# Kernel tuning notes

Measured on AMD Instinct MI355X. Metric: run time of the kernel, lower is better.

## Reference

```python
import jax, jax.numpy as jnp
import numpy as np

P, C, L, D_IN, F = 200000, 50000, 8, 64, 32


def gru_step(x, h, Wi, Wh, bi, bh):
    # torch nn.GRU single-layer cell math. Wi, Wh: [3F, F]; bi, bh: [3F]
    gi = x @ Wi.T + bi
    gh = h @ Wh.T + bh
    i_r, i_z, i_n = jnp.split(gi, 3, axis=-1)
    h_r, h_z, h_n = jnp.split(gh, 3, axis=-1)
    r = jax.nn.sigmoid(i_r + h_r)
    z = jax.nn.sigmoid(i_z + h_z)
    n = jnp.tanh(i_n + r * h_n)
    return (1.0 - z) * n + z * h


def setup_inputs() -> dict:
    key = jax.random.key(0)
    ks = jax.random.split(key, 16)
    s = 0.1
    return {
        "path_raw": jax.random.normal(ks[0], (P, D_IN), jnp.float32),
        "channel_raw": jax.random.normal(ks[1], (C, D_IN), jnp.float32),
        "path_channel_idx": jax.random.randint(ks[2], (P, L), 0, C),
        "path_lengths": jax.random.randint(ks[3], (P,), 0, L),  # valid length = lengths+1 in [1, L]
        "num_steps": 5,
        "W_path_init": s * jax.random.normal(ks[4], (D_IN, F), jnp.float32),
        "b_path_init": jnp.zeros((F,), jnp.float32),
        "W_chan_init": s * jax.random.normal(ks[5], (D_IN, F), jnp.float32),
        "b_chan_init": jnp.zeros((F,), jnp.float32),
        "Wi1": s * jax.random.normal(ks[6], (3 * F, F), jnp.float32),
        "Wh1": s * jax.random.normal(ks[7], (3 * F, F), jnp.float32),
        "bi1": jnp.zeros((3 * F,), jnp.float32),
        "bh1": jnp.zeros((3 * F,), jnp.float32),
        "Wi2": s * jax.random.normal(ks[8], (3 * F, F), jnp.float32),
        "Wh2": s * jax.random.normal(ks[9], (3 * F, F), jnp.float32),
        "bi2": jnp.zeros((3 * F,), jnp.float32),
        "bh2": jnp.zeros((3 * F,), jnp.float32),
    }


def reference(path_raw, channel_raw, path_channel_idx, path_lengths, num_steps,
              W_path_init, b_path_init, W_chan_init, b_chan_init,
              Wi1, Wh1, bi1, bh1, Wi2, Wh2, bi2, bh2):
    # Initialization: Linear + ReLU on raw padded features
    p = jax.nn.relu(path_raw @ W_path_init + b_path_init)      # [P, F]
    c = jax.nn.relu(channel_raw @ W_chan_init + b_chan_init)   # [C, F]

    # mask[p, t] = 1 if slot t is a real channel on path p (lengths in 1..L)
    mask = (jnp.arange(L)[None, :] <= path_lengths[:, None]).astype(p.dtype)  # [P, L]
    flat_idx = path_channel_idx.reshape(-1)                    # [P*L]

    for _ in range(num_steps):
        # --- GRUCell1: each path runs its channel sequence through a GRU,
        # with the path feature as the evolving hidden state. Batched over
        # all paths; masked positions keep the previous hidden state.
        def body(h, t):
            x = c[path_channel_idx[:, t]]                      # [P, F] gather
            h_new = gru_step(x, h, Wi1, Wh1, bi1, bh1)
            m = mask[:, t][:, None]
            return m * h_new + (1.0 - m) * h, None

        p, _ = jax.lax.scan(body, p, jnp.arange(L))

        # --- GRUCell2: each channel sums the features of paths containing it,
        # then does one GRU step with that sum as input, channel feat as hidden.
        contrib = (p[:, None, :] * mask[:, :, None]).reshape(P * L, F)
        agg = jax.ops.segment_sum(contrib, flat_idx, num_segments=C)  # [C, F]
        c = gru_step(agg, c, Wi2, Wh2, bi2, bh2)

    return p, c
```

## Files before the change

### kernel.cpp

```cpp
#include <hip/hip_runtime.h>

#define DIN 64
#define FF 32
#define MAX_OUTER 8
#define NCH 3

__device__ __forceinline__ float sigm(float x) {
  return 1.0f / (1.0f + __expf(-x));
}
__device__ __forceinline__ float tanh_fast(float x) {
  float e = __expf(2.0f * x);
  return 1.0f - 2.0f / (e + 1.0f);
}

template <int K>
__device__ __forceinline__ void swz_fma3(float h,
                                         const float* __restrict__ wr,
                                         const float* __restrict__ wz,
                                         const float* __restrict__ wn,
                                         float& ar, float& az, float& an) {
  if constexpr (K < FF) {
    float hk = __int_as_float(
        __builtin_amdgcn_ds_swizzle(__float_as_int(h), (K << 5)));
    ar = fmaf(hk, wr[K], ar);
    az = fmaf(hk, wz[K], az);
    an = fmaf(hk, wn[K], an);
    swz_fma3<K + 1>(h, wr, wz, wn, ar, az, an);
  }
}

template <int K, int NC>
__device__ __forceinline__ void swz_fma_multi(
    const float* __restrict__ h,
    const float* __restrict__ wr, const float* __restrict__ wz,
    const float* __restrict__ wn,
    float* __restrict__ ar, float* __restrict__ az, float* __restrict__ an) {
  if constexpr (K < FF) {
    float hk[NC];
#pragma unroll
    for (int c = 0; c < NC; ++c)
      hk[c] = __int_as_float(
          __builtin_amdgcn_ds_swizzle(__float_as_int(h[c]), (K << 5)));
#pragma unroll
    for (int c = 0; c < NC; ++c) {
      ar[c] = fmaf(hk[c], wr[K], ar[c]);
      az[c] = fmaf(hk[c], wz[K], az[c]);
      an[c] = fmaf(hk[c], wn[K], an[c]);
    }
    swz_fma_multi<K + 1, NC>(h, wr, wz, wn, ar, az, an);
  }
}

__device__ __forceinline__ int iread(const void* src, long i, int is64) {
  return is64 ? (int)((const long long*)src)[i] : ((const int*)src)[i];
}

__global__ void detect_dtypes(const int* __restrict__ idx_raw,
                              const int* __restrict__ lens_raw,
                              int* __restrict__ flags) {
  __shared__ int zi, zl;
  if (threadIdx.x == 0) { zi = 0; zl = 0; }
  __syncthreads();
  int j = threadIdx.x;
  if (idx_raw[2 * j + 1] == 0)  atomicAdd(&zi, 1);
  if (lens_raw[2 * j + 1] == 0) atomicAdd(&zl, 1);
  __syncthreads();
  if (threadIdx.x == 0) {
    flags[0] = (zi >= 250) ? 1 : 0;
    flags[1] = (zl >= 250) ? 1 : 0;
  }
}

__device__ __forceinline__ void gru_gates(
    const float* __restrict__ Wi, const float* __restrict__ Wh,
    const float* __restrict__ bi, const float* __restrict__ bh,
    const float* __restrict__ x, float* __restrict__ h) {
  float hn[FF];
#pragma unroll
  for (int g = 0; g < FF; ++g) {
    float ar   = bi[g] + bh[g];
    float az   = bi[FF + g] + bh[FF + g];
    float an_i = bi[2 * FF + g];
    float an_h = bh[2 * FF + g];
#pragma unroll
    for (int k = 0; k < FF; ++k) {
      const float xk = x[k];
      const float hk = h[k];
      ar   = fmaf(xk, Wi[g * FF + k], ar);
      ar   = fmaf(hk, Wh[g * FF + k], ar);
      az   = fmaf(xk, Wi[(FF + g) * FF + k], az);
      az   = fmaf(hk, Wh[(FF + g) * FF + k], az);
      an_i = fmaf(xk, Wi[(2 * FF + g) * FF + k], an_i);
      an_h = fmaf(hk, Wh[(2 * FF + g) * FF + k], an_h);
    }
    float r = sigm(ar);
    float z = sigm(az);
    float n = tanh_fast(fmaf(r, an_h, an_i));
    hn[g] = fmaf(z, h[g] - n, n);
  }
#pragma unroll
  for (int g = 0; g < FF; ++g) h[g] = hn[g];
}

__global__ __launch_bounds__(256) void init_proj(
    const float* __restrict__ raw,
    const float* __restrict__ W, const float* __restrict__ b,
    float* __restrict__ out, int nrows) {
  int i = blockIdx.x * blockDim.x + threadIdx.x;
  if (i >= nrows) return;
  float x[DIN];
  const float4* rp = (const float4*)(raw + (size_t)i * DIN);
#pragma unroll
  for (int q = 0; q < DIN / 4; ++q) {
    float4 v = rp[q];
    x[q * 4 + 0] = v.x; x[q * 4 + 1] = v.y; x[q * 4 + 2] = v.z; x[q * 4 + 3] = v.w;
  }
  float acc[FF];
#pragma unroll
  for (int j = 0; j < FF; ++j) acc[j] = b[j];
#pragma unroll
  for (int k = 0; k < DIN; ++k) {
    float xk = x[k];
#pragma unroll
    for (int j = 0; j < FF; ++j) acc[j] = fmaf(xk, W[k * FF + j], acc[j]);
  }
  float4* op = (float4*)(out + (size_t)i * FF);
#pragma unroll
  for (int j = 0; j < FF; j += 4) {
    float4 v;
    v.x = fmaxf(acc[j + 0], 0.0f);
    v.y = fmaxf(acc[j + 1], 0.0f);
    v.z = fmaxf(acc[j + 2], 0.0f);
    v.w = fmaxf(acc[j + 3], 0.0f);
    op[j / 4] = v;
  }
}


__global__ __launch_bounds__(256) void path_pre(
    const void* __restrict__ idx_raw, const void* __restrict__ lens_raw,
    const int* __restrict__ flags, int* __restrict__ cnt,
    int* __restrict__ lhist, int P, int C, int L) {
  __shared__ int bh[72];
  const int nb = L + 1;
  if (threadIdx.x < nb) bh[threadIdx.x] = 0;
  __syncthreads();
  int i = blockIdx.x * blockDim.x + threadIdx.x;
  if (i < P) {
    int i64 = flags[0], l64 = flags[1];
    int len = iread(lens_raw, i, l64);
    if (len > L - 1) len = L - 1;
    int lb = (len < 0) ? 0 : len;
    atomicAdd(&bh[lb], 1);
    for (int t = 0; t <= len; ++t) {
      int ch = iread(idx_raw, (long)i * L + t, i64);
      if (ch < 0) ch = 0;
      if (ch >= C) ch = C - 1;
      atomicAdd(&cnt[ch], 1);
    }
  }
  __syncthreads();
  if (threadIdx.x < nb && bh[threadIdx.x] > 0)
    atomicAdd(&lhist[threadIdx.x], bh[threadIdx.x]);
}

__global__ __launch_bounds__(1024) void scan_counts(
    const int* __restrict__ cnt, int* __restrict__ rowstart,
    int* __restrict__ cursor, int n) {
  __shared__ int buf[1024];
  __shared__ int carry;
  if (threadIdx.x == 0) carry = 0;
  __syncthreads();
  for (int base = 0; base < n; base += 1024) {
    int i = base + threadIdx.x;
    int v = (i < n) ? cnt[i] : 0;
    buf[threadIdx.x] = v;
    __syncthreads();
    for (int off = 1; off < 1024; off <<= 1) {
      int t = (threadIdx.x >= off) ? buf[threadIdx.x - off] : 0;
      __syncthreads();
      buf[threadIdx.x] += t;
      __syncthreads();
    }
    int excl = buf[threadIdx.x] - v;
    if (i < n) { rowstart[i] = carry + excl; cursor[i] = carry + excl; }
    __syncthreads();
    if (threadIdx.x == 0) carry += buf[1023];
    __syncthreads();
  }
  if (threadIdx.x == 0) rowstart[n] = carry;
}

__global__ __launch_bounds__(256) void fill_entries(
    const void* __restrict__ idx_raw, const void* __restrict__ lens_raw,
    const int* __restrict__ flags, int* __restrict__ cursor,
    int* __restrict__ entries, int P, int C, int L) {
  int i = blockIdx.x * blockDim.x + threadIdx.x;
  if (i >= P) return;
  int i64 = flags[0], l64 = flags[1];
  int len = iread(lens_raw, i, l64);
  if (len > L - 1) len = L - 1;
  for (int t = 0; t <= len; ++t) {
    int ch = iread(idx_raw, (long)i * L + t, i64);
    if (ch < 0) ch = 0;
    if (ch >= C) ch = C - 1;
    int slot = atomicAdd(&cursor[ch], 1);
    entries[slot] = i;
  }
}

__global__ __launch_bounds__(256) void fill_order2(
    const void* __restrict__ lens_raw, const int* __restrict__ flags,
    int* __restrict__ lcursor, int* __restrict__ order, int P, int L) {
  __shared__ int bh[72];
  __shared__ int bbase[72];
  const int nb = L + 1;
  if (threadIdx.x < nb) bh[threadIdx.x] = 0;
  __syncthreads();
  int i = blockIdx.x * blockDim.x + threadIdx.x;
  int lb = 0, rank = 0;
  if (i < P) {
    int len = iread(lens_raw, i, flags[1]);
    if (len > L - 1) len = L - 1;
    lb = (len < 0) ? 0 : len;
    rank = atomicAdd(&bh[lb], 1);
  }
  __syncthreads();
  if (threadIdx.x < nb && bh[threadIdx.x] > 0)
    bbase[threadIdx.x] = atomicAdd(&lcursor[threadIdx.x], bh[threadIdx.x]);
  __syncthreads();
  if (i < P) order[bbase[lb] + rank] = i;
}

__global__ __launch_bounds__(256) void build_sorted(
    const void* __restrict__ idx_raw, const void* __restrict__ lens_raw,
    const int* __restrict__ flags, const int* __restrict__ order,
    int* __restrict__ idx_s, int* __restrict__ len_s, int P, int C, int L) {
  int tid = blockIdx.x * blockDim.x + threadIdx.x;
  if (tid >= P) return;
  int i = order[tid];
  int i64 = flags[0], l64 = flags[1];
  int len = iread(lens_raw, i, l64);
  if (len > L - 1) len = L - 1;
  len_s[tid] = len;
  for (int t = 0; t < L; ++t) {
    int ch = iread(idx_raw, (long)i * L + t, i64);
    if (ch < 0) ch = 0;
    if (ch >= C) ch = C - 1;
    idx_s[(size_t)t * P + tid] = ch * (3 * FF * 4);
  }
}


__global__ __launch_bounds__(256) void gates_pre(
    const float* __restrict__ c_state,
    const float* __restrict__ Wi1, const float* __restrict__ bi1,
    const float* __restrict__ Wh2, const float* __restrict__ bh2,
    float* __restrict__ gi1, float* __restrict__ gh2, int C,
    const int* __restrict__ ns_ptr, int use_mem, int s) {
  int ns = use_mem ? *ns_ptr : 5;
  if (ns < 1 || ns > MAX_OUTER) ns = 5;
  if (s >= ns) return;
  int c = blockIdx.x * blockDim.x + threadIdx.x;
  if (c >= C) return;
  int q = blockIdx.y;
  int qq = (q < 3) ? q : q - 3;
  const float* W = ((q < 3) ? Wi1 : Wh2) + (size_t)qq * FF * FF;
  const float* b = ((q < 3) ? bi1 : bh2) + qq * FF;
  float* out = ((q < 3) ? gi1 : gh2) + (size_t)c * (3 * FF) + qq * FF;

  float x[FF];
  const float4* cp = (const float4*)(c_state + (size_t)c * FF);
#pragma unroll
  for (int t = 0; t < FF / 4; ++t) {
    float4 v = cp[t];
    x[4 * t + 0] = v.x; x[4 * t + 1] = v.y; x[4 * t + 2] = v.z; x[4 * t + 3] = v.w;
  }
  float acc[FF];
#pragma unroll
  for (int j = 0; j < FF; ++j) acc[j] = b[j];
#pragma unroll
  for (int k = 0; k < FF; ++k) {
    float xk = x[k];
#pragma unroll
    for (int j = 0; j < FF; ++j) acc[j] = fmaf(xk, W[(size_t)j * FF + k], acc[j]);
  }
  float4* op = (float4*)out;
#pragma unroll
  for (int j = 0; j < FF; j += 4) {
    float4 v; v.x = acc[j]; v.y = acc[j + 1]; v.z = acc[j + 2]; v.w = acc[j + 3];
    op[j / 4] = v;
  }
}

__global__ __launch_bounds__(256, 4) void path_step(
    const float* __restrict__ c_state, float* __restrict__ p_state,
    const void* __restrict__ idx_raw, const void* __restrict__ lens_raw,
    const int* __restrict__ flags, const int* __restrict__ order,
    const float* __restrict__ Wi, const float* __restrict__ Wh,
    const float* __restrict__ bi, const float* __restrict__ bh,
    int P, int C, int L, const int* __restrict__ ns_ptr, int use_mem, int s) {
  int ns = use_mem ? *ns_ptr : 5;
  if (ns < 1 || ns > MAX_OUTER) ns = 5;
  if (s >= ns) return;
  int tid = blockIdx.x * blockDim.x + threadIdx.x;
  if (tid >= P) return;
  int i = order[tid];
  int i64 = flags[0], l64 = flags[1];
  int len = iread(lens_raw, i, l64);
  if (len > L - 1) len = L - 1;

  float h[FF];
  const float4* pp = (const float4*)(p_state + (size_t)i * FF);
#pragma unroll
  for (int q = 0; q < FF / 4; ++q) {
    float4 v = pp[q];
    h[q * 4 + 0] = v.x; h[q * 4 + 1] = v.y; h[q * 4 + 2] = v.z; h[q * 4 + 3] = v.w;
  }

#pragma unroll 1
  for (int t = 0; t <= len && t < L; ++t) {
    int ch = iread(idx_raw, (long)i * L + t, i64);
    if (ch < 0) ch = 0;
    if (ch >= C) ch = C - 1;
    float x[FF];
    const float4* cp = (const float4*)(c_state + (size_t)ch * FF);
#pragma unroll
    for (int q = 0; q < FF / 4; ++q) {
      float4 v = cp[q];
      x[q * 4 + 0] = v.x; x[q * 4 + 1] = v.y; x[q * 4 + 2] = v.z; x[q * 4 + 3] = v.w;
    }
    gru_gates(Wi, Wh, bi, bh, x, h);
  }

  float4* op = (float4*)(p_state + (size_t)i * FF);
#pragma unroll
  for (int q = 0; q < FF / 4; ++q) {
    float4 v;
    v.x = h[q * 4 + 0]; v.y = h[q * 4 + 1]; v.z = h[q * 4 + 2]; v.w = h[q * 4 + 3];
    op[q] = v;
  }
}

__global__ __launch_bounds__(256, 3) void path_step6(
    const float* __restrict__ gi1,
    float* __restrict__ p_state,
    const int* __restrict__ idx_s,
    const int* __restrict__ len_s,
    const int* __restrict__ order,
    const float* __restrict__ Wh,
    const float* __restrict__ bh,
    int P, int L,
    const int* __restrict__ ns_ptr, int use_mem, int s) {
  int ns = use_mem ? *ns_ptr : 5;
  if (ns < 1 || ns > MAX_OUTER) ns = 5;
  if (s >= ns) return;
  const int lane = threadIdx.x & 63;
  const int g = lane & 31;
  const long wv = (long)blockIdx.x * (blockDim.x >> 6) + (threadIdx.x >> 6);
  const long base = wv * (2 * NCH);

  long pos[NCH];
  bool valid[NCH];
  int path[NCH], len[NCH];
#pragma unroll
  for (int c = 0; c < NCH; ++c) {
    pos[c] = base + 2 * c + (lane >> 5);
    valid[c] = pos[c] < P;
    if (!valid[c]) pos[c] = P - 1;
    path[c] = order[pos[c]];
    len[c] = valid[c] ? len_s[pos[c]] : -1;
  }

  float wr[FF], wz[FF], wn[FF];
  {
    const float4* a = (const float4*)(Wh + (size_t)g * FF);
    const float4* b = (const float4*)(Wh + (size_t)(FF + g) * FF);
    const float4* c = (const float4*)(Wh + (size_t)(2 * FF + g) * FF);
#pragma unroll
    for (int q = 0; q < FF / 4; ++q) {
      float4 va = a[q];
      wr[4 * q + 0] = va.x; wr[4 * q + 1] = va.y; wr[4 * q + 2] = va.z; wr[4 * q + 3] = va.w;
      float4 vb = b[q];
      wz[4 * q + 0] = vb.x; wz[4 * q + 1] = vb.y; wz[4 * q + 2] = vb.z; wz[4 * q + 3] = vb.w;
      float4 vc = c[q];
      wn[4 * q + 0] = vc.x; wn[4 * q + 1] = vc.y; wn[4 * q + 2] = vc.z; wn[4 * q + 3] = vc.w;
    }
  }
#pragma unroll
  for (int k = 0; k < FF; ++k) {
    asm volatile("" : "+v"(wr[k]), "+v"(wz[k]), "+v"(wn[k]));
  }
  const float bhr = bh[g], bhz = bh[FF + g], bhn = bh[2 * FF + g];

  float h[NCH];
#pragma unroll
  for (int c = 0; c < NCH; ++c) h[c] = p_state[(size_t)path[c] * FF + g];

  int lenM = len[0];
#pragma unroll
  for (int c = 1; c < NCH; ++c) lenM = (len[c] > lenM) ? len[c] : lenM;

  if (lenM >= 0) {
    const char* gB = (const char*)gi1 + (size_t)(4 * g);
    const int* row = idx_s;
    int off[NCH];
#pragma unroll
    for (int c = 0; c < NCH; ++c) off[c] = row[pos[c]];
    row += P;

#pragma unroll 1
    for (int t = 0; t <= lenM; ++t) {
      int offn[NCH];
#pragma unroll
      for (int c = 0; c < NCH; ++c)
        offn[c] = (t < lenM) ? row[pos[c]] : off[c];
      row += P;

      float gr[NCH], gz[NCH], gn[NCH];
#pragma unroll
      for (int c = 0; c < NCH; ++c) {
        const char* p = gB + off[c];
        gr[c] = *(const float*)(p);
        gz[c] = *(const float*)(p + 128);
        gn[c] = *(const float*)(p + 256);
      }

      float ar[NCH], az[NCH], an[NCH];
#pragma unroll
      for (int c = 0; c < NCH; ++c) { ar[c] = bhr; az[c] = bhz; an[c] = bhn; }
      swz_fma_multi<0, NCH>(h, wr, wz, wn, ar, az, an);

#pragma unroll
      for (int c = 0; c < NCH; ++c) {
        float r = sigm(gr[c] + ar[c]);
        float z = sigm(gz[c] + az[c]);
        float n = tanh_fast(fmaf(r, an[c], gn[c]));
        float hn_ = fmaf(z, h[c] - n, n);
        h[c] = (t <= len[c]) ? hn_ : h[c];
        off[c] = offn[c];
      }
    }
  }
#pragma unroll
  for (int c = 0; c < NCH; ++c)
    if (valid[c]) p_state[(size_t)path[c] * FF + g] = h[c];
}

__global__ __launch_bounds__(256) void agg_gather(
    const float* __restrict__ p_state, const int* __restrict__ rowstart,
    const int* __restrict__ entries, float* __restrict__ agg,
    int C, const int* __restrict__ ns_ptr, int use_mem, int s) {
  int ns = use_mem ? *ns_ptr : 5;
  if (ns < 1 || ns > MAX_OUTER) ns = 5;
  if (s >= ns) return;
  int c = blockIdx.x * 8 + (threadIdx.x >> 5);
  int j = threadIdx.x & 31;
  if (c >= C) return;
  int rs = rowstart[c], re = rowstart[c + 1];
  float acc = 0.0f, acc2 = 0.0f;
  int e = rs;
  for (; e + 1 < re; e += 2) {
    int p0 = entries[e], p1 = entries[e + 1];
    acc  += p_state[(size_t)p0 * FF + j];
    acc2 += p_state[(size_t)p1 * FF + j];
  }
  if (e < re) acc += p_state[(size_t)entries[e] * FF + j];
  agg[(size_t)c * FF + j] = acc + acc2;
}

__global__ __launch_bounds__(256) void chan_step(
    float* __restrict__ c_state, const float* __restrict__ agg,
    const float* __restrict__ Wi, const float* __restrict__ Wh,
    const float* __restrict__ bi, const float* __restrict__ bh,
    int C, const int* __restrict__ ns_ptr, int use_mem, int s) {
  int ns = use_mem ? *ns_ptr : 5;
  if (ns < 1 || ns > MAX_OUTER) ns = 5;
  if (s >= ns) return;
  int i = blockIdx.x * blockDim.x + threadIdx.x;
  if (i >= C) return;

  float x[FF], h[FF];
  const float4* apv = (const float4*)(agg + (size_t)i * FF);
  const float4* cpv = (const float4*)(c_state + (size_t)i * FF);
#pragma unroll
  for (int q = 0; q < FF / 4; ++q) {
    float4 a = apv[q];
    x[q * 4 + 0] = a.x; x[q * 4 + 1] = a.y; x[q * 4 + 2] = a.z; x[q * 4 + 3] = a.w;
    float4 c = cpv[q];
    h[q * 4 + 0] = c.x; h[q * 4 + 1] = c.y; h[q * 4 + 2] = c.z; h[q * 4 + 3] = c.w;
  }
  gru_gates(Wi, Wh, bi, bh, x, h);
  float4* op = (float4*)(c_state + (size_t)i * FF);
#pragma unroll
  for (int q = 0; q < FF / 4; ++q) {
    float4 v;
    v.x = h[q * 4 + 0]; v.y = h[q * 4 + 1]; v.z = h[q * 4 + 2]; v.w = h[q * 4 + 3];
    op[q] = v;
  }
}

__global__ __launch_bounds__(256, 3) void chan_fused(
    float* __restrict__ c_state, const float* __restrict__ p_state,
    const int* __restrict__ rowstart, const int* __restrict__ entries,
    const float* __restrict__ gh2,
    const float* __restrict__ Wi2, const float* __restrict__ bi2,
    int C, const int* __restrict__ ns_ptr, int use_mem, int s) {
  int ns = use_mem ? *ns_ptr : 5;
  if (ns < 1 || ns > MAX_OUTER) ns = 5;
  if (s >= ns) return;
  const int lane = threadIdx.x & 63;
  const int g = lane & 31;
  const long wv = (long)blockIdx.x * (blockDim.x >> 6) + (threadIdx.x >> 6);
  const long c = wv * 2 + (lane >> 5);
  if (c >= C) return;

  float wr[FF], wz[FF], wn[FF];
  {
    const float4* a = (const float4*)(Wi2 + (size_t)g * FF);
    const float4* b = (const float4*)(Wi2 + (size_t)(FF + g) * FF);
    const float4* d = (const float4*)(Wi2 + (size_t)(2 * FF + g) * FF);
#pragma unroll
    for (int q = 0; q < FF / 4; ++q) {
      float4 va = a[q];
      wr[4 * q + 0] = va.x; wr[4 * q + 1] = va.y; wr[4 * q + 2] = va.z; wr[4 * q + 3] = va.w;
      float4 vb = b[q];
      wz[4 * q + 0] = vb.x; wz[4 * q + 1] = vb.y; wz[4 * q + 2] = vb.z; wz[4 * q + 3] = vb.w;
      float4 vd = d[q];
      wn[4 * q + 0] = vd.x; wn[4 * q + 1] = vd.y; wn[4 * q + 2] = vd.z; wn[4 * q + 3] = vd.w;
    }
  }
  const float bir = bi2[g], biz = bi2[FF + g], bin_ = bi2[2 * FF + g];

  int rs = rowstart[c], re = rowstart[c + 1];
  float acc = 0.0f, acc2 = 0.0f;
  int e = rs;
  for (; e + 3 < re; e += 4) {
    int p0 = entries[e], p1 = entries[e + 1], p2 = entries[e + 2], p3 = entries[e + 3];
    acc  += p_state[(size_t)p0 * FF + g];
    acc2 += p_state[(size_t)p1 * FF + g];
    acc  += p_state[(size_t)p2 * FF + g];
    acc2 += p_state[(size_t)p3 * FF + g];
  }
  for (; e < re; ++e) acc += p_state[(size_t)entries[e] * FF + g];
  float x = acc + acc2;

  float ar = bir, az = biz, an = bin_;
  swz_fma3<0>(x, wr, wz, wn, ar, az, an);
  const float* pre = gh2 + (size_t)c * (3 * FF);
  float hr = pre[g], hz = pre[FF + g], hn = pre[2 * FF + g];
  float h = c_state[(size_t)c * FF + g];
  float r = sigm(ar + hr);
  float z = sigm(az + hz);
  float n = tanh_fast(fmaf(r, hn, an));
  c_state[(size_t)c * FF + g] = fmaf(z, h - n, n);
}

__global__ void beacon(float* out, int code) {
  out[0] = (float)(1024 * (64 + code));
}

extern "C" void kernel_launch(void* const* d_in, const int* in_sizes, int n_in,
                              void* d_out, int out_size, void* d_ws, size_t ws_size,
                              hipStream_t stream) {
  int base = 5, use_mem = 1;
  if (n_in == 16) { base = 4; use_mem = 0; }
  const float* path_raw = (const float*)d_in[0];
  const float* chan_raw = (const float*)d_in[1];
  const void* idx_raw  = d_in[2];
  const void* lens_raw = d_in[3];
  const int* ns_ptr = use_mem ? (const int*)d_in[4] : (const int*)d_in[0];
  const float* Wp  = (const float*)d_in[base + 0];
  const float* bp  = (const float*)d_in[base + 1];
  const float* Wc  = (const float*)d_in[base + 2];
  const float* bc  = (const float*)d_in[base + 3];
  const float* Wi1 = (const float*)d_in[base + 4];
  const float* Wh1 = (const float*)d_in[base + 5];
  const float* bi1 = (const float*)d_in[base + 6];
  const float* bh1 = (const float*)d_in[base + 7];
  const float* Wi2 = (const float*)d_in[base + 8];
  const float* Wh2 = (const float*)d_in[base + 9];
  const float* bi2 = (const float*)d_in[base + 10];
  const float* bh2 = (const float*)d_in[base + 11];

  long P = in_sizes[0] / DIN;
  long C = in_sizes[1] / DIN;
  long L = (P > 0) ? (in_sizes[2] / P) : 8;
  long PL = P * L;

  int anomaly = 0;
  if (n_in != 17 && n_in != 16) anomaly |= 1;
  if (P <= 0 || C <= 0 || L < 1 || L > 64) anomaly |= 2;
  if (P > 0 && in_sizes[3] != (int)P) anomaly |= 4;
  if ((long)out_size != (P + C) * FF) anomaly |= 8;

  float* out_f   = (float*)d_out;
  float* p_state = out_f;
  float* c_state = out_f + (size_t)P * FF;

  int* flags    = (int*)d_ws;
  int* rowstart = flags + 16;
  int* cursor   = rowstart + (C + 1);
  int* entries  = cursor + C;
  float* agg    = (float*)(entries + PL);
  int* order    = (int*)(agg + (size_t)C * FF);
  int* lhist    = order + P;
  int* lrow     = lhist + (L + 1);
  size_t base_words = (size_t)16 + (C + 1) + C + PL + (size_t)C * FF +
                      P + (L + 1) + (L + 2);
  size_t w1 = (base_words + 3) & ~(size_t)3;
  int* idx_s = (int*)d_ws + w1;
  int* len_s = idx_s + PL;
  size_t w2 = (w1 + (size_t)PL + P + 3) & ~(size_t)3;
  float* gi1 = (float*)d_ws + w2;
  float* gh2 = gi1 + (size_t)C * 3 * FF;
  size_t need_old = base_words * 4;
  size_t need_new = (w2 + (size_t)2 * C * 3 * FF) * 4;
  if (ws_size < need_old) anomaly |= 16;
  int use_new = (!anomaly) && (ws_size >= need_new) && (L >= 1) && (L <= 8) &&
                (C < 5000000);

  detect_dtypes<<<1, 256, 0, stream>>>((const int*)idx_raw, (const int*)lens_raw, flags);

  init_proj<<<(int)((P + 255) / 256), 256, 0, stream>>>(path_raw, Wp, bp, p_state, (int)P);
  init_proj<<<(int)((C + 255) / 256), 256, 0, stream>>>(chan_raw, Wc, bc, c_state, (int)C);

  (void)hipMemsetAsync(cursor, 0, (size_t)C * sizeof(int), stream);
  (void)hipMemsetAsync(lhist, 0, (size_t)(L + 1) * sizeof(int), stream);
  path_pre<<<(int)((P + 255) / 256), 256, 0, stream>>>(
      idx_raw, lens_raw, flags, cursor, lhist, (int)P, (int)C, (int)L);
  scan_counts<<<1, 1024, 0, stream>>>(cursor, rowstart, cursor, (int)C);
  fill_entries<<<(int)((P + 255) / 256), 256, 0, stream>>>(
      idx_raw, lens_raw, flags, cursor, entries, (int)P, (int)C, (int)L);
  scan_counts<<<1, 1024, 0, stream>>>(lhist, lrow, lhist, (int)L + 1);
  fill_order2<<<(int)((P + 255) / 256), 256, 0, stream>>>(
      lens_raw, flags, lhist, order, (int)P, (int)L);

  if (use_new) {
    build_sorted<<<(int)((P + 255) / 256), 256, 0, stream>>>(
        idx_raw, lens_raw, flags, order, idx_s, len_s, (int)P, (int)C, (int)L);
    const int paths_per_block = 4 * 2 * NCH;
    for (int s = 0; s < MAX_OUTER; ++s) {
      dim3 gpre((unsigned)((C + 255) / 256), 6, 1);
      gates_pre<<<gpre, 256, 0, stream>>>(
          c_state, Wi1, bi1, Wh2, bh2, gi1, gh2, (int)C, ns_ptr, use_mem, s);
      path_step6<<<(int)((P + paths_per_block - 1) / paths_per_block), 256, 0, stream>>>(
          gi1, p_state, idx_s, len_s, order, Wh1, bh1, (int)P, (int)L,
          ns_ptr, use_mem, s);
      chan_fused<<<(int)((C + 7) / 8), 256, 0, stream>>>(
          c_state, p_state, rowstart, entries, gh2, Wi2, bi2, (int)C,
          ns_ptr, use_mem, s);
    }
  } else {
    for (int s = 0; s < MAX_OUTER; ++s) {
      path_step<<<(int)((P + 255) / 256), 256, 0, stream>>>(
          c_state, p_state, idx_raw, lens_raw, flags, order,
          Wi1, Wh1, bi1, bh1, (int)P, (int)C, (int)L, ns_ptr, use_mem, s);
      agg_gather<<<(int)((C + 7) / 8), 256, 0, stream>>>(
          p_state, rowstart, entries, agg, (int)C, ns_ptr, use_mem, s);
      chan_step<<<(int)((C + 255) / 256), 256, 0, stream>>>(
          c_state, agg, Wi2, Wh2, bi2, bh2, (int)C, ns_ptr, use_mem, s);
    }
  }

  if (anomaly) beacon<<<1, 1, 0, stream>>>(out_f, anomaly);
}
```

Baseline: 1.911 ms.

## Parallelize channel count scan, fuse entry fill into sorted build, raise NCH

```diff
diff --git a/kernel.cpp b/kernel.cpp
--- a/kernel.cpp
+++ b/kernel.cpp
@@ -3,7 +3,7 @@
 #define DIN 64
 #define FF 32
 #define MAX_OUTER 8
-#define NCH 3
+#define NCH 4
 
 __device__ __forceinline__ float sigm(float x) {
   return 1.0f / (1.0f + __expf(-x));
@@ -189,6 +189,51 @@
     __syncthreads();
   }
   if (threadIdx.x == 0) rowstart[n] = carry;
+}
+
+__global__ __launch_bounds__(1024) void scan_blk(
+    const int* __restrict__ cnt, int* __restrict__ rowstart,
+    int* __restrict__ partials, int n) {
+  __shared__ int buf[1024];
+  int i = blockIdx.x * 1024 + threadIdx.x;
+  int v = (i < n) ? cnt[i] : 0;
+  buf[threadIdx.x] = v;
+  __syncthreads();
+  for (int off = 1; off < 1024; off <<= 1) {
+    int t = (threadIdx.x >= off) ? buf[threadIdx.x - off] : 0;
+    __syncthreads();
+    buf[threadIdx.x] += t;
+    __syncthreads();
+  }
+  if (i < n) rowstart[i] = buf[threadIdx.x] - v;
+  if (threadIdx.x == 1023) partials[blockIdx.x] = buf[1023];
+}
+
+__global__ __launch_bounds__(1024) void scan_part(
+    int* __restrict__ partials, int* __restrict__ total_out, int nb) {
+  __shared__ int buf[1024];
+  int v = (threadIdx.x < nb) ? partials[threadIdx.x] : 0;
+  buf[threadIdx.x] = v;
+  __syncthreads();
+  for (int off = 1; off < 1024; off <<= 1) {
+    int t = (threadIdx.x >= off) ? buf[threadIdx.x - off] : 0;
+    __syncthreads();
+    buf[threadIdx.x] += t;
+    __syncthreads();
+  }
+  if (threadIdx.x < nb) partials[threadIdx.x] = buf[threadIdx.x] - v;
+  if (threadIdx.x == 1023) *total_out = buf[1023];
+}
+
+__global__ __launch_bounds__(1024) void scan_add(
+    int* __restrict__ rowstart, int* __restrict__ cursor,
+    const int* __restrict__ partials, int n) {
+  int i = blockIdx.x * 1024 + threadIdx.x;
+  if (i < n) {
+    int v = rowstart[i] + partials[blockIdx.x];
+    rowstart[i] = v;
+    cursor[i] = v;
+  }
 }
 
 __global__ __launch_bounds__(256) void fill_entries(
@@ -232,9 +277,10 @@
   if (i < P) order[bbase[lb] + rank] = i;
 }
 
-__global__ __launch_bounds__(256) void build_sorted(
+__global__ __launch_bounds__(256) void build_sorted2(
     const void* __restrict__ idx_raw, const void* __restrict__ lens_raw,
     const int* __restrict__ flags, const int* __restrict__ order,
+    int* __restrict__ cursor, int* __restrict__ entries,
     int* __restrict__ idx_s, int* __restrict__ len_s, int P, int C, int L) {
   int tid = blockIdx.x * blockDim.x + threadIdx.x;
   if (tid >= P) return;
@@ -248,6 +294,10 @@
     if (ch < 0) ch = 0;
     if (ch >= C) ch = C - 1;
     idx_s[(size_t)t * P + tid] = ch * (3 * FF * 4);
+    if (t <= len) {
+      int slot = atomicAdd(&cursor[ch], 1);
+      entries[slot] = i;
+    }
   }
 }
 
@@ -614,11 +664,13 @@
   size_t w2 = (w1 + (size_t)PL + P + 3) & ~(size_t)3;
   float* gi1 = (float*)d_ws + w2;
   float* gh2 = gi1 + (size_t)C * 3 * FF;
+  int* partials = (int*)(gh2 + (size_t)C * 3 * FF);
+  long nbC = (C + 1023) / 1024;
   size_t need_old = base_words * 4;
-  size_t need_new = (w2 + (size_t)2 * C * 3 * FF) * 4;
+  size_t need_new = (w2 + (size_t)2 * C * 3 * FF + nbC + 2) * 4;
   if (ws_size < need_old) anomaly |= 16;
   int use_new = (!anomaly) && (ws_size >= need_new) && (L >= 1) && (L <= 8) &&
-                (C < 5000000);
+                (C < 5000000) && (nbC <= 1024);
 
   detect_dtypes<<<1, 256, 0, stream>>>((const int*)idx_raw, (const int*)lens_raw, flags);
 
@@ -629,16 +681,17 @@
   (void)hipMemsetAsync(lhist, 0, (size_t)(L + 1) * sizeof(int), stream);
   path_pre<<<(int)((P + 255) / 256), 256, 0, stream>>>(
       idx_raw, lens_raw, flags, cursor, lhist, (int)P, (int)C, (int)L);
-  scan_counts<<<1, 1024, 0, stream>>>(cursor, rowstart, cursor, (int)C);
-  fill_entries<<<(int)((P + 255) / 256), 256, 0, stream>>>(
-      idx_raw, lens_raw, flags, cursor, entries, (int)P, (int)C, (int)L);
-  scan_counts<<<1, 1024, 0, stream>>>(lhist, lrow, lhist, (int)L + 1);
-  fill_order2<<<(int)((P + 255) / 256), 256, 0, stream>>>(
-      lens_raw, flags, lhist, order, (int)P, (int)L);
 
   if (use_new) {
-    build_sorted<<<(int)((P + 255) / 256), 256, 0, stream>>>(
-        idx_raw, lens_raw, flags, order, idx_s, len_s, (int)P, (int)C, (int)L);
+    scan_blk<<<(int)nbC, 1024, 0, stream>>>(cursor, rowstart, partials, (int)C);
+    scan_part<<<1, 1024, 0, stream>>>(partials, rowstart + C, (int)nbC);
+    scan_add<<<(int)nbC, 1024, 0, stream>>>(rowstart, cursor, partials, (int)C);
+    scan_counts<<<1, 1024, 0, stream>>>(lhist, lrow, lhist, (int)L + 1);
+    fill_order2<<<(int)((P + 255) / 256), 256, 0, stream>>>(
+        lens_raw, flags, lhist, order, (int)P, (int)L);
+    build_sorted2<<<(int)((P + 255) / 256), 256, 0, stream>>>(
+        idx_raw, lens_raw, flags, order, cursor, entries, idx_s, len_s,
+        (int)P, (int)C, (int)L);
     const int paths_per_block = 4 * 2 * NCH;
     for (int s = 0; s < MAX_OUTER; ++s) {
       dim3 gpre((unsigned)((C + 255) / 256), 6, 1);
@@ -652,6 +705,12 @@
           ns_ptr, use_mem, s);
     }
   } else {
+    scan_counts<<<1, 1024, 0, stream>>>(cursor, rowstart, cursor, (int)C);
+    fill_entries<<<(int)((P + 255) / 256), 256, 0, stream>>>(
+        idx_raw, lens_raw, flags, cursor, entries, (int)P, (int)C, (int)L);
+    scan_counts<<<1, 1024, 0, stream>>>(lhist, lrow, lhist, (int)L + 1);
+    fill_order2<<<(int)((P + 255) / 256), 256, 0, stream>>>(
+        lens_raw, flags, lhist, order, (int)P, (int)L);
     for (int s = 0; s < MAX_OUTER; ++s) {
       path_step<<<(int)((P + 255) / 256), 256, 0, stream>>>(
           c_state, p_state, idx_raw, lens_raw, flags, order,
```

After: 1.742 ms. 8.8% less time.
